# Optimization experiments

Hardware: AMD Instinct MI355X
Metric: run time of the kernel (lower is better)

Reference implementation:

```python
import jax, jax.numpy as jnp
import numpy as np

N_EMBD = 1024
N_HEAD = 16


def setup_inputs() -> dict:
    key = jax.random.key(0)
    ks = jax.random.split(key, 11)
    B, T, T2, C = 4, 2048, 1024, N_EMBD
    s = 0.02
    return {
        "x": jax.random.normal(ks[0], (B, T, C), jnp.float32),
        "enc_x": jax.random.normal(ks[1], (B, T2, C), jnp.float32),
        "Wq": jax.random.normal(ks[2], (C, C), jnp.float32) * s,
        "bq": jax.random.normal(ks[3], (C,), jnp.float32) * s,
        "Wk": jax.random.normal(ks[4], (C, C), jnp.float32) * s,
        "bk": jax.random.normal(ks[5], (C,), jnp.float32) * s,
        "Wv": jax.random.normal(ks[6], (C, C), jnp.float32) * s,
        "bv": jax.random.normal(ks[7], (C,), jnp.float32) * s,
        "Wo": jax.random.normal(ks[8], (C, C), jnp.float32) * s,
        "bo": jax.random.normal(ks[9], (C,), jnp.float32) * s,
    }


def reference(x, enc_x, Wq, bq, Wk, bk, Wv, bv, Wo, bo):
    B, T, C = x.shape
    B2, T2, C2 = enc_x.shape
    H = N_HEAD
    D = C // H  # head dim
    q = x @ Wq + bq          # [B,T,C]
    k = enc_x @ Wk + bk      # [B,T2,C]
    v = enc_x @ Wv + bv      # [B,T2,C]
    q = q.reshape(B, T, H, D).transpose(0, 2, 1, 3)    # [B,H,T,D]
    k = k.reshape(B2, T2, H, D).transpose(0, 2, 1, 3)  # [B,H,T2,D]
    v = v.reshape(B2, T2, H, D).transpose(0, 2, 1, 3)  # [B,H,T2,D]
    att = jnp.einsum("bhtd,bhsd->bhts", q, k) * (1.0 / jnp.sqrt(jnp.float32(D)))
    att = jax.nn.softmax(att, axis=-1)                 # [B,H,T,T2]
    y = jnp.einsum("bhts,bhsd->bhtd", att, v)          # [B,H,T,D]
    y = y.transpose(0, 2, 1, 3).reshape(B, T, C)
    return y @ Wo + bo
```

## Files before the change

kernel.cpp:

```cpp
#include <hip/hip_runtime.h>
#include <hip/hip_bf16.h>


typedef __bf16 bf16_t;
typedef __bf16 bf16x8 __attribute__((ext_vector_type(8)));
typedef float f32x4 __attribute__((ext_vector_type(4)));
typedef float f32x16 __attribute__((ext_vector_type(16)));
typedef unsigned int u32x4 __attribute__((ext_vector_type(4)));

#define AS1C(p) ((const __attribute__((address_space(1))) void*)(p))
#define AS3(p)  ((__attribute__((address_space(3))) void*)(p))

constexpr int CC  = 1024;
constexpr int TT  = 2048;
constexpr int TT2 = 1024;

#if __has_builtin(__builtin_amdgcn_exp2f)
__device__ __forceinline__ float EXP2(float x) { return __builtin_amdgcn_exp2f(x); }
#else
__device__ __forceinline__ float EXP2(float x) { return exp2f(x); }
#endif

__global__ void cast2(const float* __restrict__ in0, bf16_t* __restrict__ out0, int n0,
                      const float* __restrict__ in1, bf16_t* __restrict__ out1, int n1) {
    int i = blockIdx.x * blockDim.x + threadIdx.x;
    int stride = gridDim.x * blockDim.x;
    for (; i < n0 + n1; i += stride) {
        const float* in = (i < n0) ? in0 : in1;
        bf16_t* out = (i < n0) ? out0 : out1;
        int j = (i < n0) ? i : i - n0;
        const float4* p = (const float4*)in + 2 * (size_t)j;
        float4 a = p[0], b = p[1];
        bf16x8 v;
        v[0] = (bf16_t)a.x; v[1] = (bf16_t)a.y; v[2] = (bf16_t)a.z; v[3] = (bf16_t)a.w;
        v[4] = (bf16_t)b.x; v[5] = (bf16_t)b.y; v[6] = (bf16_t)b.z; v[7] = (bf16_t)b.w;
        *(bf16x8*)(out + (size_t)j * 8) = v;
    }
}

__global__ __launch_bounds__(256) void transW(const float* __restrict__ W0, const float* __restrict__ W1,
                                              const float* __restrict__ W2, const float* __restrict__ W3,
                                              bf16_t* __restrict__ T0, bf16_t* __restrict__ T1,
                                              bf16_t* __restrict__ T2, bf16_t* __restrict__ T3) {
    __shared__ float tile[32][33];
    const float* W; bf16_t* Tt;
    switch (blockIdx.z) {
        case 0:  W = W0; Tt = T0; break;
        case 1:  W = W1; Tt = T1; break;
        case 2:  W = W2; Tt = T2; break;
        default: W = W3; Tt = T3; break;
    }
    int x = threadIdx.x & 31, y = threadIdx.x >> 5;
    int bx = blockIdx.x * 32, by = blockIdx.y * 32;
    for (int i = 0; i < 4; ++i) {
        int r = y + i * 8;
        tile[r][x] = W[(size_t)(by + r) * 1024 + bx + x];
    }
    __syncthreads();
    for (int i = 0; i < 4; ++i) {
        int r = y + i * 8;
        Tt[(size_t)(bx + r) * 1024 + by + x] = (bf16_t)tile[x][r];
    }
}

template<bool OUT_BF16, bool SPLIT>
__device__ __forceinline__ void gemm_body(bf16_t* As, bf16_t* Bs,
                                          const bf16_t* __restrict__ A,
                                          const bf16_t* __restrict__ Bt,
                                          const float* __restrict__ biasA,
                                          const float* __restrict__ biasB,
                                          void* __restrict__ outA,
                                          void* __restrict__ outB,
                                          float scale, int lgNT, int mband, int bid) {
    const int tid  = threadIdx.x;
    const int lane = tid & 63;
    const int wave = tid >> 6;
    const int wr = wave >> 1, wc = wave & 1;
    const int l15 = lane & 15, lhi = lane >> 4;

    const int xcd = bid & 7;
    const int j   = bid >> 3;
    const int n0  = (j & ((1 << lgNT) - 1)) * 128;
    const int m0  = (xcd * mband + (j >> lgNT)) * 128;

    f32x4 acc[4][4] = {};

    for (int k0 = 0; k0 < 1024; k0 += 32) {
        for (int i = 0; i < 2; ++i) {
            int e   = i * 2048 + wave * 512 + lane * 8;
            int row = e >> 5, col = e & 31;
            __builtin_amdgcn_global_load_lds(AS1C(A  + (size_t)(m0 + row) * 1024 + k0 + col),
                                             AS3(As + i * 2048 + wave * 512), 16, 0, 0);
            __builtin_amdgcn_global_load_lds(AS1C(Bt + (size_t)(n0 + row) * 1024 + k0 + col),
                                             AS3(Bs + i * 2048 + wave * 512), 16, 0, 0);
        }
        __syncthreads();
        bf16x8 a[4], b[4];
        #pragma unroll
        for (int m = 0; m < 4; ++m)
            a[m] = *(const bf16x8*)&As[(wr * 64 + m * 16 + l15) * 32 + lhi * 8];
        #pragma unroll
        for (int n = 0; n < 4; ++n)
            b[n] = *(const bf16x8*)&Bs[(wc * 64 + n * 16 + l15) * 32 + lhi * 8];
        #pragma unroll
        for (int m = 0; m < 4; ++m)
            #pragma unroll
            for (int n = 0; n < 4; ++n)
                acc[m][n] = __builtin_amdgcn_mfma_f32_16x16x32_bf16(a[m], b[n], acc[m][n], 0, 0, 0);
        __syncthreads();
    }

    #pragma unroll
    for (int n = 0; n < 4; ++n) {
        int col = n0 + wc * 64 + n * 16 + l15;
        const float* bias = biasA;
        void* out = outA;
        if (SPLIT && col >= 1024) { bias = biasB; out = outB; col -= 1024; }
        float bv = bias[col];
        #pragma unroll
        for (int m = 0; m < 4; ++m) {
            int rowb = m0 + wr * 64 + m * 16 + lhi * 4;
            #pragma unroll
            for (int r = 0; r < 4; ++r) {
                float v = (acc[m][n][r] + bv) * scale;
                if (OUT_BF16)
                    ((bf16_t*)out)[(size_t)(rowb + r) * 1024 + col] = (bf16_t)v;
                else
                    ((float*)out)[(size_t)(rowb + r) * 1024 + col] = v;
            }
        }
    }
}

__global__ __launch_bounds__(256) void gemm_qkv(const bf16_t* __restrict__ xb,
                                                const bf16_t* __restrict__ eb,
                                                const bf16_t* __restrict__ wtq,
                                                const bf16_t* __restrict__ wtk,
                                                const float* __restrict__ bq,
                                                const float* __restrict__ bk,
                                                const float* __restrict__ bv,
                                                bf16_t* __restrict__ Qs,
                                                bf16_t* __restrict__ Ks,
                                                bf16_t* __restrict__ Vs,
                                                float qscale) {
    __shared__ __align__(16) bf16_t As[128 * 32];
    __shared__ __align__(16) bf16_t Bs[128 * 32];
    int bid = blockIdx.x;
    if (bid < 512)
        gemm_body<true, false>(As, Bs, xb, wtq, bq, nullptr, (void*)Qs, nullptr,
                               qscale, 3, 8, bid);
    else
        gemm_body<true, true>(As, Bs, eb, wtk, bk, bv, (void*)Ks, (void*)Vs,
                              1.0f, 4, 4, bid - 512);
}

__global__ __launch_bounds__(256) void gemm_out(const bf16_t* __restrict__ yb,
                                                const bf16_t* __restrict__ wto,
                                                const float* __restrict__ bo,
                                                float* __restrict__ out) {
    __shared__ __align__(16) bf16_t As[128 * 32];
    __shared__ __align__(16) bf16_t Bs[128 * 32];
    gemm_body<false, false>(As, Bs, yb, wto, bo, nullptr, (void*)out, nullptr,
                            1.0f, 3, 8, blockIdx.x);
}

__global__ __launch_bounds__(256) void vtrans(const bf16_t* __restrict__ Vs, bf16_t* __restrict__ Vt) {
    __shared__ bf16_t t[64][72];
    int bh = blockIdx.y, b = bh >> 4, h = bh & 15;
    int kv0 = blockIdx.x * 64;
    int r = threadIdx.x >> 2, c0 = (threadIdx.x & 3) * 16;
    const bf16_t* src = Vs + (size_t)(b * 1024 + kv0 + r) * 1024 + h * 64 + c0;
    *(bf16x8*)&t[r][c0]     = *(const bf16x8*)src;
    *(bf16x8*)&t[r][c0 + 8] = *(const bf16x8*)(src + 8);
    __syncthreads();
    int d = threadIdx.x >> 2, k0 = (threadIdx.x & 3) * 16;
    bf16x8 v0, v1;
    #pragma unroll
    for (int j = 0; j < 8; ++j) { v0[j] = t[k0 + j][d]; v1[j] = t[k0 + 8 + j][d]; }
    bf16_t* dst = Vt + ((size_t)bh * 64 + d) * 1024 + kv0 + k0;
    *(bf16x8*)dst       = v0;
    *(bf16x8*)(dst + 8) = v1;
}

__device__ __forceinline__ unsigned pk_bf16(float lo, float hi) {
    unsigned r;
    asm("v_cvt_pk_bf16_f32 %0, %1, %2" : "=v"(r) : "v"(lo), "v"(hi));
    return r;
}
__device__ __forceinline__ void swap32(unsigned &a, unsigned &b) {
    asm("v_permlane32_swap_b32 %0, %1" : "+v"(a), "+v"(b));
}
__device__ __forceinline__ float sum_halves(float x) {
    unsigned a = __builtin_bit_cast(unsigned, x), b = a;
    swap32(a, b);
    return __builtin_bit_cast(float, a) + __builtin_bit_cast(float, b);
}
__device__ __forceinline__ bf16x8 ldsf(const bf16_t* base, int row, int colb) {
    int off = row * 128 + (colb ^ ((row & 7) << 4));
    return *(const bf16x8*)((const char*)base + off);
}
__device__ __forceinline__ bf16x8 packP(const f32x16& s0, const f32x16& s1, int kt) {
    const f32x16& sp = (kt < 2) ? s0 : s1;
    const int rb = (kt & 1) * 8;
    unsigned a0 = pk_bf16(sp[rb + 0], sp[rb + 1]);
    unsigned a1 = pk_bf16(sp[rb + 2], sp[rb + 3]);
    unsigned a2 = pk_bf16(sp[rb + 4], sp[rb + 5]);
    unsigned a3 = pk_bf16(sp[rb + 6], sp[rb + 7]);
    swap32(a0, a2);
    swap32(a1, a3);
    union { u32x4 u; bf16x8 h; } cv;
    cv.u = (u32x4){a0, a1, a2, a3};
    return cv.h;
}

__global__ __launch_bounds__(256, 2) void attn256(const bf16_t* __restrict__ Q,
                                                  const bf16_t* __restrict__ K,
                                                  const bf16_t* __restrict__ Vt,
                                                  bf16_t* __restrict__ Y) {
    __shared__ __align__(16) bf16_t SM[3][2][64 * 64];

    const int tid = threadIdx.x;
    const int l   = tid & 63;
    const int w   = tid >> 6;
    const int l31 = l & 31;
    const int lh  = l >> 5;

    const int bid = blockIdx.x;
    const int bh  = bid & 63;
    const int qb  = bid >> 6;
    const int b = bh >> 4, h = bh & 15;
    const int q0 = qb * 256 + w * 64;

    const bf16_t* Qb = Q + (size_t)b * TT * CC + h * 64;
    const char* Kc = (const char*)(K + (size_t)b * TT2 * CC + h * 64);
    const char* Vc = (const char*)(Vt + (size_t)bh * 64 * 1024);

    bf16x8 qfA[4], qfB[4];
    #pragma unroll
    for (int kt = 0; kt < 4; ++kt) {
        qfA[kt] = *(const bf16x8*)&Qb[(size_t)(q0 + l31)      * CC + kt * 16 + lh * 8];
        qfB[kt] = *(const bf16x8*)&Qb[(size_t)(q0 + 32 + l31) * CC + kt * 16 + lh * 8];
    }
    __builtin_amdgcn_sched_barrier(0);

    f32x16 yA0 = {}, yA1 = {}, yB0 = {}, yB1 = {};
    float lsA = 0.f, lsB = 0.f;

    const int krow = w * 16 + (l >> 3);
    const int ss   = ((l & 7) ^ (l >> 3)) & 7;
    const int off0 = krow * 2048 + ss * 16;
    const int off1 = off0 + 8 * 2048;

    #define STAGE(t, buf)                                                                 \
        do {                                                                              \
            __builtin_amdgcn_global_load_lds(AS1C(Kc + (size_t)(t) * 131072 + off0),      \
                                             AS3((char*)&SM[buf][0][0] + w * 2048), 16, 0, 0);        \
            __builtin_amdgcn_global_load_lds(AS1C(Kc + (size_t)(t) * 131072 + off1),      \
                                             AS3((char*)&SM[buf][0][0] + w * 2048 + 1024), 16, 0, 0); \
            __builtin_amdgcn_global_load_lds(AS1C(Vc + (t) * 128 + off0),                 \
                                             AS3((char*)&SM[buf][1][0] + w * 2048), 16, 0, 0);        \
            __builtin_amdgcn_global_load_lds(AS1C(Vc + (t) * 128 + off1),                 \
                                             AS3((char*)&SM[buf][1][0] + w * 2048 + 1024), 16, 0, 0); \
        } while (0)

    #define SUMEXP(s0, s1, ls)                                                    \
        do {                                                                      \
            float rs = 0.f;                                                       \
            _Pragma("unroll")                                                     \
            for (int r = 0; r < 16; ++r) {                                        \
                s0[r] = EXP2(s0[r]);                                              \
                s1[r] = EXP2(s1[r]);                                              \
                rs += s0[r] + s1[r];                                              \
            }                                                                     \
            ls += sum_halves(rs);                                                 \
        } while (0)

    constexpr int NT = TT2 / 64;
    STAGE(0, 0);
    STAGE(1, 1);

    int cur = 0;
    for (int t = 0; t < NT; ++t) {
        if (t + 1 < NT) asm volatile("s_waitcnt vmcnt(4)" ::: "memory");
        else            asm volatile("s_waitcnt vmcnt(0)" ::: "memory");
        __builtin_amdgcn_sched_barrier(0);
        __builtin_amdgcn_s_barrier();
        __builtin_amdgcn_sched_barrier(0);

        if (t + 2 < NT) {
            int nb = cur + 2; if (nb >= 3) nb -= 3;
            STAGE(t + 2, nb);
        }

        const bf16_t* Kl = &SM[cur][0][0];
        const bf16_t* Vl = &SM[cur][1][0];

        f32x16 sA0 = {}, sA1 = {}, sB0 = {}, sB1 = {};
        #pragma unroll
        for (int kt = 0; kt < 4; ++kt) {
            int colb = kt * 32 + (lh << 4);
            bf16x8 a0 = ldsf(Kl, l31,      colb);
            bf16x8 a1 = ldsf(Kl, 32 + l31, colb);
            sA0 = __builtin_amdgcn_mfma_f32_32x32x16_bf16(a0, qfA[kt], sA0, 0, 0, 0);
            sB0 = __builtin_amdgcn_mfma_f32_32x32x16_bf16(a0, qfB[kt], sB0, 0, 0, 0);
            sA1 = __builtin_amdgcn_mfma_f32_32x32x16_bf16(a1, qfA[kt], sA1, 0, 0, 0);
            sB1 = __builtin_amdgcn_mfma_f32_32x32x16_bf16(a1, qfB[kt], sB1, 0, 0, 0);
        }

        SUMEXP(sA0, sA1, lsA);
        SUMEXP(sB0, sB1, lsB);

        __builtin_amdgcn_s_setprio(1);
        #pragma unroll
        for (int kt = 0; kt < 4; ++kt) {
            bf16x8 pA = packP(sA0, sA1, kt);
            bf16x8 pB = packP(sB0, sB1, kt);
            int colb = kt * 32 + (lh << 4);
            bf16x8 v0 = ldsf(Vl, l31,      colb);
            bf16x8 v1 = ldsf(Vl, 32 + l31, colb);
            yA0 = __builtin_amdgcn_mfma_f32_32x32x16_bf16(v0, pA, yA0, 0, 0, 0);
            yA1 = __builtin_amdgcn_mfma_f32_32x32x16_bf16(v1, pA, yA1, 0, 0, 0);
            yB0 = __builtin_amdgcn_mfma_f32_32x32x16_bf16(v0, pB, yB0, 0, 0, 0);
            yB1 = __builtin_amdgcn_mfma_f32_32x32x16_bf16(v1, pB, yB1, 0, 0, 0);
        }
        __builtin_amdgcn_s_setprio(0);

        ++cur; if (cur == 3) cur = 0;
    }
    #undef STAGE
    #undef SUMEXP

    __syncthreads();

    float iA = 1.f / lsA, iB = 1.f / lsB;
    char* ob = (char*)&SM[0][0][0] + w * 8192;
    const int sw = (l31 & 7) << 4;
    #pragma unroll
    for (int r = 0; r < 16; ++r) {
        int drow = (r & 3) + 8 * (r >> 2) + 4 * lh;
        *(bf16_t*)(ob + l31 * 128 + ((drow * 2) ^ sw))               = (bf16_t)(yA0[r] * iA);
        *(bf16_t*)(ob + l31 * 128 + (((32 + drow) * 2) ^ sw))        = (bf16_t)(yA1[r] * iA);
        *(bf16_t*)(ob + 4096 + l31 * 128 + ((drow * 2) ^ sw))        = (bf16_t)(yB0[r] * iB);
        *(bf16_t*)(ob + 4096 + l31 * 128 + (((32 + drow) * 2) ^ sw)) = (bf16_t)(yB1[r] * iB);
    }
    __syncthreads();
    bf16_t* Yb = Y + (size_t)b * TT * CC + h * 64 + (size_t)q0 * CC;
    #pragma unroll
    for (int i = 0; i < 8; ++i) {
        int qr = i * 8 + (l >> 3);
        int c  = ((l & 7) * 16) ^ ((qr & 7) << 4);
        bf16x8 v = *(const bf16x8*)(ob + (qr >> 5) * 4096 + (qr & 31) * 128 + c);
        *(bf16x8*)&Yb[(size_t)qr * CC + (l & 7) * 8] = v;
    }
}

extern "C" void kernel_launch(void* const* d_in, const int* in_sizes, int n_in,
                              void* d_out, int out_size, void* d_ws, size_t ws_size,
                              hipStream_t stream) {
    const float* x   = (const float*)d_in[0];
    const float* enc = (const float*)d_in[1];
    const float* Wq  = (const float*)d_in[2];
    const float* bq  = (const float*)d_in[3];
    const float* Wk  = (const float*)d_in[4];
    const float* bk  = (const float*)d_in[5];
    const float* Wv  = (const float*)d_in[6];
    const float* bv  = (const float*)d_in[7];
    const float* Wo  = (const float*)d_in[8];
    const float* bo  = (const float*)d_in[9];

    char* w = (char*)d_ws;
    size_t o = 0;
    bf16_t* xb  = (bf16_t*)(w + o); o += (size_t)8192 * 1024 * 2;
    bf16_t* eb  = (bf16_t*)(w + o); o += (size_t)4096 * 1024 * 2;
    bf16_t* wtq = (bf16_t*)(w + o); o += (size_t)1024 * 1024 * 2;
    bf16_t* wtk = (bf16_t*)(w + o); o += (size_t)1024 * 1024 * 2;
    bf16_t* wtv = (bf16_t*)(w + o); o += (size_t)1024 * 1024 * 2;
    bf16_t* wto = (bf16_t*)(w + o); o += (size_t)1024 * 1024 * 2;
    bf16_t* Qs  = (bf16_t*)(w + o); o += (size_t)8192 * 1024 * 2;
    bf16_t* Ks  = (bf16_t*)(w + o); o += (size_t)4096 * 1024 * 2;
    bf16_t* Vs  = (bf16_t*)(w + o); o += (size_t)4096 * 1024 * 2;
    bf16_t* yb  = (bf16_t*)(w + o); o += (size_t)8192 * 1024 * 2;
    bf16_t* Vt  = eb;

    cast2<<<2048, 256, 0, stream>>>(x, xb, 8192 * 1024 / 8, enc, eb, 4096 * 1024 / 8);
    transW<<<dim3(32, 32, 4), 256, 0, stream>>>(Wq, Wk, Wv, Wo, wtq, wtk, wtv, wto);

    const float qscale = 0.125f * 1.4426950408889634f;
    gemm_qkv<<<1024, 256, 0, stream>>>(xb, eb, wtq, wtk, bq, bk, bv, Qs, Ks, Vs, qscale);

    vtrans<<<dim3(16, 64), 256, 0, stream>>>(Vs, Vt);

    attn256<<<512, 256, 0, stream>>>(Qs, Ks, Vt, yb);

    gemm_out<<<512, 256, 0, stream>>>(yb, wto, bo, (float*)d_out);
}
```

Before: 139.9 us.

## Replace QKV projection GEMM with 256x256-tile, 8-wave, double-buffered pipelined kernel

Replaces the 128x128-tile QKV GEMM with a new kernel that uses 256x256 output tiles, 512 threads, and 128 KB of double-buffered LDS filled via global_load_lds. Reads use an XOR swizzle, and prefetch is interleaved with MFMA phases, using explicit waitcnt, barriers and setprio. The goal is more data reuse per tile, overlap of global loads with compute, and fewer LDS bank conflicts. The cost is higher register and LDS pressure, with only 256 blocks, which risks underfilling the GPU. The old templated GEMM body is reduced to serve only the fp32 output projection.

```diff
diff --git a/kernel.cpp b/kernel.cpp
--- a/kernel.cpp
+++ b/kernel.cpp
@@ -63,15 +63,164 @@
     }
 }
 
-template<bool OUT_BF16, bool SPLIT>
+
+#define SB0 __builtin_amdgcn_sched_barrier(0)
+#define GLL(src, dst) __builtin_amdgcn_global_load_lds(AS1C(src), AS3(dst), 16, 0, 0)
+
+__device__ __forceinline__ bf16x8 ldx(const char* p) { return *(const bf16x8*)p; }
+
+__global__ __launch_bounds__(512, 2) void gemm_qkv8(const bf16_t* __restrict__ xb,
+                                                    const bf16_t* __restrict__ eb,
+                                                    const bf16_t* __restrict__ wtq,
+                                                    const bf16_t* __restrict__ wtk,
+                                                    const float* __restrict__ bq,
+                                                    const float* __restrict__ bk,
+                                                    const float* __restrict__ bv,
+                                                    bf16_t* __restrict__ Qs,
+                                                    bf16_t* __restrict__ Ks,
+                                                    bf16_t* __restrict__ Vs,
+                                                    float qscale) {
+    __shared__ __align__(16) char GLDS[131072];
+    char* ldsA = &GLDS[0];
+    char* ldsB = &GLDS[65536];
+
+    const int tid = threadIdx.x;
+    const int w   = tid >> 6;
+    const int l   = tid & 63;
+    const int wm  = w >> 2;
+    const int wn  = w & 3;
+    const int l15 = l & 15, lhi = l >> 4;
+
+    const int bid = blockIdx.x;
+    const bf16_t* Ap; const bf16_t* Bp;
+    int m0, n0;
+    float scale;
+    const float* bias; bf16_t* outp; int outn0;
+    if (bid < 128) {
+        int xcd = bid & 7, j = bid >> 3;
+        n0 = (j & 3) * 256; m0 = (xcd * 4 + (j >> 2)) * 256;
+        Ap = xb; Bp = wtq; scale = qscale;
+        bias = bq; outp = Qs; outn0 = n0;
+    } else {
+        int b2 = bid - 128;
+        int xcd = b2 & 7, j = b2 >> 3;
+        n0 = (j & 7) * 256; m0 = (xcd * 2 + (j >> 3)) * 256;
+        Ap = eb; Bp = wtk; scale = 1.0f;
+        if (n0 < 1024) { bias = bk; outp = Ks; outn0 = n0; }
+        else           { bias = bv; outp = Vs; outn0 = n0 - 1024; }
+    }
+
+    const int lrow  = l >> 3;
+    const int lslot = (l & 7) ^ lrow;
+    const char* Asrc = (const char*)(Ap + (size_t)(m0 + w * 16 + lrow) * 1024 + lslot * 8);
+    const char* Bsrc = (const char*)(Bp + (size_t)(n0 + w * 16 + lrow) * 1024 + lslot * 8);
+    #define STG_A(t, buf, h)                                                                   \
+        do {                                                                                   \
+            GLL(Asrc + (size_t)(h) * 262144 + (t) * 128,         ldsA + (buf) * 32768 + (h) * 16384 + w * 2048);        \
+            GLL(Asrc + (size_t)(h) * 262144 + 16384 + (t) * 128, ldsA + (buf) * 32768 + (h) * 16384 + w * 2048 + 1024); \
+        } while (0)
+    #define STG_B(t, buf, h)                                                                   \
+        do {                                                                                   \
+            GLL(Bsrc + (size_t)(h) * 262144 + (t) * 128,         ldsB + (buf) * 32768 + (h) * 16384 + w * 2048);        \
+            GLL(Bsrc + (size_t)(h) * 262144 + 16384 + (t) * 128, ldsB + (buf) * 32768 + (h) * 16384 + w * 2048 + 1024); \
+        } while (0)
+
+    const int aoff = (wm * 128 + l15) * 128;
+    const int boff = (wn * 64 + l15) * 128;
+    const int sl0  = ((0 + lhi) ^ (l15 & 7)) << 4;
+    const int sl1  = ((4 + lhi) ^ (l15 & 7)) << 4;
+
+    #define RD_A(dst, KA, qm)                                                    \
+        do { _Pragma("unroll") for (int mf = 0; mf < 4; ++mf) {                  \
+            dst[mf * 2 + 0] = ldx((KA) + aoff + ((qm) * 64 + mf * 16) * 128 + sl0); \
+            dst[mf * 2 + 1] = ldx((KA) + aoff + ((qm) * 64 + mf * 16) * 128 + sl1); } } while (0)
+    #define RD_B(dst, KB, qn)                                                    \
+        do { _Pragma("unroll") for (int nf = 0; nf < 2; ++nf) {                  \
+            dst[nf * 2 + 0] = ldx((KB) + boff + ((qn) * 32 + nf * 16) * 128 + sl0); \
+            dst[nf * 2 + 1] = ldx((KB) + boff + ((qn) * 32 + nf * 16) * 128 + sl1); } } while (0)
+
+    #define MFMA16(qm, qn, Af, Bf)                                                             \
+        do { __builtin_amdgcn_s_setprio(1);                                                    \
+            _Pragma("unroll") for (int mf = 0; mf < 4; ++mf)                                   \
+            _Pragma("unroll") for (int nf = 0; nf < 2; ++nf) {                                 \
+                acc[(qm) * 4 + mf][(qn) * 2 + nf] = __builtin_amdgcn_mfma_f32_16x16x32_bf16(   \
+                    Af[mf * 2 + 0], Bf[nf * 2 + 0], acc[(qm) * 4 + mf][(qn) * 2 + nf], 0, 0, 0); \
+                acc[(qm) * 4 + mf][(qn) * 2 + nf] = __builtin_amdgcn_mfma_f32_16x16x32_bf16(   \
+                    Af[mf * 2 + 1], Bf[nf * 2 + 1], acc[(qm) * 4 + mf][(qn) * 2 + nf], 0, 0, 0); } \
+            __builtin_amdgcn_s_setprio(0); } while (0)
+
+    #define PH_BAR do { SB0; __builtin_amdgcn_s_barrier(); SB0;                                \
+                        asm volatile("s_waitcnt lgkmcnt(0)" ::: "memory"); SB0; } while (0)
+    #define PH_END do { SB0; __builtin_amdgcn_s_barrier(); SB0; } while (0)
+
+    f32x4 acc[8][4] = {};
+    bf16x8 A0[8], A1[8], B0[4], B1[4];
+
+    STG_A(0, 0, 0); STG_A(0, 0, 1);
+    STG_B(0, 0, 0); STG_B(0, 0, 1);
+    STG_A(1, 1, 0); STG_A(1, 1, 1);
+    asm volatile("s_waitcnt vmcnt(4)" ::: "memory");
+    SB0; __builtin_amdgcn_s_barrier(); SB0;
+
+    constexpr int NT = 16;
+    for (int t = 0; t < NT; ++t) {
+        const int buf = t & 1;
+        const char* KA = ldsA + buf * 32768;
+        const char* KB = ldsB + buf * 32768;
+
+        if (t + 1 < NT) STG_B(t + 1, buf ^ 1, 0);
+        RD_A(A0, KA, 0); RD_B(B0, KB, 0);
+        PH_BAR;
+        MFMA16(0, 0, A0, B0);
+        PH_END;
+
+        if (t + 1 < NT) STG_B(t + 1, buf ^ 1, 1);
+        RD_A(A1, KA, 1);
+        PH_BAR;
+        MFMA16(1, 0, A1, B0);
+        PH_END;
+
+        if (t + 2 < NT) STG_A(t + 2, buf, 0);
+        RD_B(B1, KB, 1);
+        PH_BAR;
+        MFMA16(1, 1, A1, B1);
+        PH_END;
+
+        if (t + 2 < NT) STG_A(t + 2, buf, 1);
+        SB0; __builtin_amdgcn_s_barrier(); SB0;
+        MFMA16(0, 1, A0, B1);
+        if (t < NT - 2) asm volatile("s_waitcnt vmcnt(4)" ::: "memory");
+        else            asm volatile("s_waitcnt vmcnt(0)" ::: "memory");
+        PH_END;
+    }
+
+    #pragma unroll
+    for (int ni = 0; ni < 4; ++ni) {
+        int col = outn0 + wn * 64 + ni * 16 + l15;
+        float bvv = bias[col];
+        #pragma unroll
+        for (int mi = 0; mi < 8; ++mi) {
+            int rowb = m0 + wm * 128 + mi * 16 + lhi * 4;
+            #pragma unroll
+            for (int r = 0; r < 4; ++r)
+                outp[(size_t)(rowb + r) * 1024 + col] = (bf16_t)((acc[mi][ni][r] + bvv) * scale);
+        }
+    }
+    #undef STG_A
+    #undef STG_B
+    #undef RD_A
+    #undef RD_B
+    #undef MFMA16
+    #undef PH_BAR
+    #undef PH_END
+}
+
 __device__ __forceinline__ void gemm_body(bf16_t* As, bf16_t* Bs,
                                           const bf16_t* __restrict__ A,
                                           const bf16_t* __restrict__ Bt,
-                                          const float* __restrict__ biasA,
-                                          const float* __restrict__ biasB,
-                                          void* __restrict__ outA,
-                                          void* __restrict__ outB,
-                                          float scale, int lgNT, int mband, int bid) {
+                                          const float* __restrict__ bias,
+                                          float* __restrict__ out,
+                                          int lgNT, int mband, int bid) {
     const int tid  = threadIdx.x;
     const int lane = tid & 63;
     const int wave = tid >> 6;
@@ -113,45 +262,15 @@
     #pragma unroll
     for (int n = 0; n < 4; ++n) {
         int col = n0 + wc * 64 + n * 16 + l15;
-        const float* bias = biasA;
-        void* out = outA;
-        if (SPLIT && col >= 1024) { bias = biasB; out = outB; col -= 1024; }
         float bv = bias[col];
         #pragma unroll
         for (int m = 0; m < 4; ++m) {
             int rowb = m0 + wr * 64 + m * 16 + lhi * 4;
             #pragma unroll
-            for (int r = 0; r < 4; ++r) {
-                float v = (acc[m][n][r] + bv) * scale;
-                if (OUT_BF16)
-                    ((bf16_t*)out)[(size_t)(rowb + r) * 1024 + col] = (bf16_t)v;
-                else
-                    ((float*)out)[(size_t)(rowb + r) * 1024 + col] = v;
-            }
+            for (int r = 0; r < 4; ++r)
+                out[(size_t)(rowb + r) * 1024 + col] = acc[m][n][r] + bv;
         }
     }
-}
-
-__global__ __launch_bounds__(256) void gemm_qkv(const bf16_t* __restrict__ xb,
-                                                const bf16_t* __restrict__ eb,
-                                                const bf16_t* __restrict__ wtq,
-                                                const bf16_t* __restrict__ wtk,
-                                                const float* __restrict__ bq,
-                                                const float* __restrict__ bk,
-                                                const float* __restrict__ bv,
-                                                bf16_t* __restrict__ Qs,
-                                                bf16_t* __restrict__ Ks,
-                                                bf16_t* __restrict__ Vs,
-                                                float qscale) {
-    __shared__ __align__(16) bf16_t As[128 * 32];
-    __shared__ __align__(16) bf16_t Bs[128 * 32];
-    int bid = blockIdx.x;
-    if (bid < 512)
-        gemm_body<true, false>(As, Bs, xb, wtq, bq, nullptr, (void*)Qs, nullptr,
-                               qscale, 3, 8, bid);
-    else
-        gemm_body<true, true>(As, Bs, eb, wtk, bk, bv, (void*)Ks, (void*)Vs,
-                              1.0f, 4, 4, bid - 512);
 }
 
 __global__ __launch_bounds__(256) void gemm_out(const bf16_t* __restrict__ yb,
@@ -160,8 +279,7 @@
                                                 float* __restrict__ out) {
     __shared__ __align__(16) bf16_t As[128 * 32];
     __shared__ __align__(16) bf16_t Bs[128 * 32];
-    gemm_body<false, false>(As, Bs, yb, wto, bo, nullptr, (void*)out, nullptr,
-                            1.0f, 3, 8, blockIdx.x);
+    gemm_body(As, Bs, yb, wto, bo, out, 3, 8, blockIdx.x);
 }
 
 __global__ __launch_bounds__(256) void vtrans(const bf16_t* __restrict__ Vs, bf16_t* __restrict__ Vt) {
@@ -386,7 +504,7 @@
     transW<<<dim3(32, 32, 4), 256, 0, stream>>>(Wq, Wk, Wv, Wo, wtq, wtk, wtv, wto);
 
     const float qscale = 0.125f * 1.4426950408889634f;
-    gemm_qkv<<<1024, 256, 0, stream>>>(xb, eb, wtq, wtk, bq, bk, bv, Qs, Ks, Vs, qscale);
+    gemm_qkv8<<<256, 512, 0, stream>>>(xb, eb, wtq, wtk, bq, bk, bv, Qs, Ks, Vs, qscale);
 
     vtrans<<<dim3(16, 64), 256, 0, stream>>>(Vs, Vt);
 
```

Measured after the change: 127.7 us. -8.7%, faster.
